# Kernel optimization log

Measured on AMD Instinct MI355X. Metric: run time of the kernel, lower is better.

The kernel has to match this reference:

```python
import jax, jax.numpy as jnp
import numpy as np

N_CLASSES = 64
K_NEIGHBORS = 10
ITERATIONS = 3
IN_DIM = 512
D_MODEL = 256
N_SUPPORT = 2048
N_QUERY = 6144


def setup_inputs() -> dict:
    key = jax.random.key(0)
    k1, k2, k3, k4 = jax.random.split(key, 4)
    support = jax.random.normal(k1, (1, N_SUPPORT, IN_DIM), dtype=jnp.float32)
    query = jax.random.normal(k2, (1, N_QUERY, IN_DIM), dtype=jnp.float32)
    support_labels = jax.random.randint(k3, (N_SUPPORT,), 0, N_CLASSES)
    W = jax.random.normal(k4, (IN_DIM, D_MODEL), dtype=jnp.float32) / np.sqrt(IN_DIM)
    return {"support": support, "query": query, "support_labels": support_labels, "W": W}


def reference(support, query, support_labels, W):
    n_way = N_CLASSES
    ns = support.shape[1]
    nq = query.shape[1]

    # encoder: linear projection
    s_emb = jnp.einsum('bnd,de->bne', support, W)   # (1, ns, D)
    q_emb = jnp.einsum('bnd,de->bne', query, W)     # (1, nq, D)
    all_emb = jnp.concatenate([s_emb, q_emb], axis=1)  # (1, n, D)

    # prototypes (computed in the original forward; unused downstream)
    onehot_s = jax.nn.one_hot(support_labels, n_way, dtype=s_emb.dtype)  # (ns, C)
    counts = onehot_s.sum(0)
    protos = (onehot_s.T @ s_emb[0]) / jnp.maximum(counts, 1.0)[:, None]

    # kNN graph via cdist + topk(smallest) + scatter
    x = all_emb[0]                                  # (n, D)
    n = x.shape[0]
    sq = jnp.sum(x * x, axis=-1)
    d2 = sq[:, None] + sq[None, :] - 2.0 * (x @ x.T)
    dist = jnp.sqrt(jnp.maximum(d2, 0.0))           # (n, n)
    k = min(K_NEIGHBORS, n - 1)
    _, idx = jax.lax.top_k(-dist, k)                # k nearest (incl. self)
    adj = jnp.zeros((n, n), dtype=jnp.float32)
    adj = adj.at[jnp.arange(n)[:, None], idx].set(1.0)
    adj = ((adj + adj.T) > 0).astype(jnp.float32)   # symmetrize

    # row-normalized transition and label propagation
    deg = adj.sum(axis=1, keepdims=True)
    deg = jnp.where(deg == 0, 1.0, deg)
    trans = adj / deg
    label_mat = jnp.concatenate(
        [onehot_s, jnp.zeros((nq, n_way), dtype=jnp.float32)], axis=0)  # (n, C)
    labels = label_mat
    for _ in range(ITERATIONS):
        labels = trans @ labels

    pred = jnp.argmax(labels, axis=-1)              # (n,)
    query_pred = pred[ns:]
    logits = jax.nn.one_hot(query_pred, n_way, dtype=jnp.float32)[None]  # (1, nq, C)
    # protos participates in the original forward; keep it live (no-op add of zeros)
    logits = logits + 0.0 * jnp.sum(protos) * 0.0
    return logits
```

## Files before the change

kernel.cpp:

```cpp
#include <hip/hip_runtime.h>
#include <stdint.h>

#define NS   2048
#define NQ   6144
#define NN   8192
#define IND  512
#define DM   256
#define KNB  10
#define NSPLIT 8
#define PCAP 1536

#define AS1 __attribute__((address_space(1)))
#define AS3 __attribute__((address_space(3)))

typedef short bf16x8 __attribute__((ext_vector_type(8)));
typedef float f32x4  __attribute__((ext_vector_type(4)));
typedef unsigned long long u64;

__device__ __forceinline__ unsigned short f2bf(float v)
{
    unsigned int u = __float_as_uint(v);
    unsigned int r = (u + 0x7fffu + ((u >> 16) & 1u)) >> 16;
    return (unsigned short)r;
}
__device__ __forceinline__ float bf2f(unsigned short h)
{
    return __uint_as_float(((unsigned int)h) << 16);
}

__device__ __forceinline__ void key_insert(u64 key, u64 K[KNB])
{
    u64 cur = key;
#pragma unroll
    for (int s = 0; s < KNB; ++s) {
        u64 lo = (cur < K[s]) ? cur : K[s];
        u64 hi = (cur < K[s]) ? K[s] : cur;
        K[s] = lo; cur = hi;
    }
}

__global__ __launch_bounds__(256) void wpack_kernel(const float* __restrict__ W,
                                                    bf16x8* __restrict__ Wthi,
                                                    bf16x8* __restrict__ Wtlo)
{
    int f = blockIdx.x * 256 + threadIdx.x;
    int dim = f & 255, qp = (f >> 8) & 3, c = f >> 10;
    int k0 = 32 * c + 8 * qp;
    bf16x8 h8, l8;
#pragma unroll
    for (int j = 0; j < 8; ++j) {
        float v = W[(size_t)(k0 + j) * DM + dim];
        unsigned short hu = f2bf(v);
        float hf = bf2f(hu);
        unsigned short lu = f2bf(v - hf);
        h8[j] = (short)hu; l8[j] = (short)lu;
    }
    Wthi[f] = h8; Wtlo[f] = l8;
}

__global__ __launch_bounds__(256) void embed_kernel(
    const float* __restrict__ support, const float* __restrict__ query,
    const bf16x8* __restrict__ Wthi, const bf16x8* __restrict__ Wtlo,
    bf16x8* __restrict__ Ghi, bf16x8* __restrict__ Glo, float* __restrict__ sq)
{
    __shared__ __align__(16) char lds[36928];
    bf16x8* Ehf = reinterpret_cast<bf16x8*>(lds);
    bf16x8* Elf = Ehf + 1024;
    float*  et  = reinterpret_cast<float*>(lds);
    float*  sqred = reinterpret_cast<float*>(lds + 32768);
    const int t = threadIdx.x;
    const int l = t & 63, w = t >> 6;
    const int lm = l & 15, q = l >> 4;
    const int i0 = blockIdx.x * 16;

    {
        const int node = t & 15;
        const int g = i0 + node;
        const float* src = (g < NS) ? (support + (size_t)g * IND)
                                    : (query + (size_t)(g - NS) * IND);
#pragma unroll
        for (int i = 0; i < 4; ++i) {
            int cq = (t >> 4) + 16 * i;
            const float* p = src + cq * 8;
            float4 v0 = *reinterpret_cast<const float4*>(p);
            float4 v1 = *reinterpret_cast<const float4*>(p + 4);
            float vv[8] = {v0.x, v0.y, v0.z, v0.w, v1.x, v1.y, v1.z, v1.w};
            bf16x8 h8, l8;
#pragma unroll
            for (int j = 0; j < 8; ++j) {
                unsigned short hu = f2bf(vv[j]);
                float hf = bf2f(hu);
                unsigned short lu = f2bf(vv[j] - hf);
                h8[j] = (short)hu; l8[j] = (short)lu;
            }
            Ehf[cq * 16 + node] = h8;
            Elf[cq * 16 + node] = l8;
        }
    }
    __syncthreads();

    f32x4 acc[4];
#pragma unroll
    for (int nt = 0; nt < 4; ++nt) acc[nt] = (f32x4){0.f, 0.f, 0.f, 0.f};
    const int dimb = 64 * w + lm;
    for (int c = 0; c < 16; ++c) {
        const bf16x8 Anh = Ehf[(c * 4 + q) * 16 + lm];
        const bf16x8 Anl = Elf[(c * 4 + q) * 16 + lm];
        const int fb = c * 1024 + q * 256 + dimb;
#pragma unroll
        for (int nt = 0; nt < 4; ++nt) {
            const bf16x8 Wh = Wthi[fb + 16 * nt];
            const bf16x8 Wl = Wtlo[fb + 16 * nt];
            f32x4 a = acc[nt];
            a = __builtin_amdgcn_mfma_f32_16x16x32_bf16(Anh, Wh, a, 0, 0, 0);
            a = __builtin_amdgcn_mfma_f32_16x16x32_bf16(Anh, Wl, a, 0, 0, 0);
            a = __builtin_amdgcn_mfma_f32_16x16x32_bf16(Anl, Wh, a, 0, 0, 0);
            a = __builtin_amdgcn_mfma_f32_16x16x32_bf16(Anl, Wl, a, 0, 0, 0);
            acc[nt] = a;
        }
    }
    __syncthreads();

#pragma unroll
    for (int r = 0; r < 4; ++r) {
        float s = 0.f;
#pragma unroll
        for (int nt = 0; nt < 4; ++nt) {
            float v = acc[nt][r];
            et[(4 * q + r) * 260 + dimb + 16 * nt] = v;
            s += v * v;
        }
        sqred[(4 * q + r) * 65 + w * 16 + lm] = s;
    }
    __syncthreads();

#pragma unroll
    for (int i = 0; i < 2; ++i) {
        int f = t + 256 * i;
        int node = f & 15, qd = (f >> 4) & 3, cd = f >> 6;
        const float* ep = &et[node * 260 + 32 * cd + 8 * qd];
        bf16x8 h8, l8;
#pragma unroll
        for (int j = 0; j < 8; ++j) {
            float v = ep[j];
            unsigned short hu = f2bf(v);
            float hf = bf2f(hu);
            unsigned short lu = f2bf(v - hf);
            h8[j] = (short)hu; l8[j] = (short)lu;
        }
        size_t gi = (size_t)(cd * 4 + qd) * NN + i0 + node;
        Ghi[gi] = h8;
        Glo[gi] = l8;
    }
    if (t < 16) {
        float s = 0.f;
#pragma unroll
        for (int x = 0; x < 64; ++x) s += sqred[t * 65 + x];
        sq[i0 + t] = s;
    }
}

__global__ __launch_bounds__(256, 2) void dist_topk_kernel(
    const bf16x8* __restrict__ Ghi, const bf16x8* __restrict__ Glo,
    const float* __restrict__ sq, u64* __restrict__ cand)
{
    __shared__ bf16x8 stage[2][1024];
    __shared__ u64 stk[4][256];
    const int t  = threadIdx.x;
    const int l  = t & 63, w = t >> 6;
    const int lm = l & 15, q = l >> 4;
    const int i0 = blockIdx.x * 64;
    const int row = i0 + 16 * w + lm;
    const int split = blockIdx.y;

    const float  sqi    = sq[row];
    const size_t rowIdx = (size_t)q * NN + row;

    u64 K[KNB];
#pragma unroll
    for (int s = 0; s < KNB; ++s) K[s] = ~0ull;
    u64 thr = ~0ull;
    u64 thr_row = ~0ull;
    int cnt = 0;

    auto drain = [&]() {
        u64 live = __ballot(cnt > 0);
        while (live) {
            if (cnt > 0) {
                --cnt;
                u64 key = stk[cnt][t];
                if (key < thr) {
                    key_insert(key, K);
                    thr = K[KNB - 1];
                }
            }
            live = __ballot(cnt > 0);
        }
    };

    auto stage_issue = [&](int it, int b) {
        const int jt = split * 8 + (it >> 3);
        const int c  = it & 7;
        const int j0 = jt * 128;
        const size_t cbase = (size_t)c * (NN * 4);
        const bool hi = (w < 2);
        const int  wf = (w & 1) * 256;
        const bf16x8* gsel = hi ? Ghi : Glo;
#pragma unroll
        for (int u = 0; u < 4; ++u) {
            const int f  = wf + u * 64;
            const int qr = f >> 7, col0 = f & 127;
            const bf16x8* g = gsel + cbase + (size_t)qr * NN + j0 + col0 + l;
            __builtin_amdgcn_global_load_lds((const AS1 void*)g,
                                             (AS3 void*)&stage[b][(hi ? 0 : 512) + f],
                                             16, 0, 0);
        }
    };

    stage_issue(0, 0);
    __syncthreads();

    f32x4 acc[8];
    for (int it = 0; it < 64; ++it) {
        const int c = it & 7;
        const int b = it & 1;
        if (it + 1 < 64) stage_issue(it + 1, (it + 1) & 1);
        if (c == 0) {
#pragma unroll
            for (int mt = 0; mt < 8; ++mt) acc[mt] = (f32x4){0.f, 0.f, 0.f, 0.f};
        }
        const size_t co = (size_t)c * (NN * 4);
        const bf16x8 Bh = Ghi[co + rowIdx];
        const bf16x8 Bl = Glo[co + rowIdx];
        const bf16x8* sh = &stage[b][0];
        const bf16x8* sl = &stage[b][512];
        const int fq = q * 128 + lm;
#pragma unroll
        for (int mt = 0; mt < 8; ++mt) {
            const int fi = fq + 16 * mt;
            const bf16x8 Ah = sh[fi];
            const bf16x8 Al = sl[fi];
            f32x4 a = acc[mt];
            a = __builtin_amdgcn_mfma_f32_16x16x32_bf16(Ah, Bh, a, 0, 0, 0);
            a = __builtin_amdgcn_mfma_f32_16x16x32_bf16(Ah, Bl, a, 0, 0, 0);
            a = __builtin_amdgcn_mfma_f32_16x16x32_bf16(Al, Bh, a, 0, 0, 0);
            a = __builtin_amdgcn_mfma_f32_16x16x32_bf16(Al, Bl, a, 0, 0, 0);
            acc[mt] = a;
        }
        if (c == 7) {
            const int j0 = split * 1024 + (it >> 3) * 128;
#pragma unroll
            for (int mt = 0; mt < 8; ++mt) {
                const int jb = j0 + 16 * mt + 4 * q;
                const f32x4 sqj = *reinterpret_cast<const f32x4*>(&sq[jb]);
#pragma unroll
                for (int r = 0; r < 4; ++r) {
                    float d2 = fmaxf(sqi + sqj[r] - 2.0f * acc[mt][r], 0.0f);
                    u64 key = ((u64)__float_as_uint(d2) << 32) | (unsigned)(jb + r);
                    if (key < thr_row) { stk[cnt][t] = key; ++cnt; }
                }
                drain();
            }
            u64 tr = K[KNB - 1];
            u64 o  = __shfl_xor(tr, 16, 64); tr = (o < tr) ? o : tr;
            o      = __shfl_xor(tr, 32, 64); tr = (o < tr) ? o : tr;
            thr_row = tr;
        }
        __syncthreads();
    }
    __syncthreads();
    u64* dump = reinterpret_cast<u64*>(&stage[0][0]);
#pragma unroll
    for (int s = 0; s < KNB; ++s) dump[t * KNB + s] = K[s];
    if (q == 0) {
#pragma unroll
        for (int qq = 1; qq < 4; ++qq)
#pragma unroll
            for (int s = 0; s < KNB; ++s) {
                u64 key = dump[(t + qq * 16) * KNB + s];
                if (key < thr) {
                    key_insert(key, K);
                    thr = K[KNB - 1];
                }
            }
        size_t base = (size_t)row * (NSPLIT * KNB) + split * KNB;
#pragma unroll
        for (int s = 0; s < KNB; ++s) cand[base + s] = K[s];
    }
}

__global__ __launch_bounds__(256) void merge_adj_kernel(
    const u64* __restrict__ cand, unsigned int* __restrict__ bits)
{
    int i = blockIdx.x * blockDim.x + threadIdx.x;
    if (i >= NN) return;
    const u64* cp = cand + (size_t)i * (NSPLIT * KNB);
    u64 K[KNB];
#pragma unroll
    for (int s = 0; s < KNB; ++s) K[s] = cp[s];
    u64 thr = K[KNB - 1];
    for (int s = KNB; s < NSPLIT * KNB; ++s) {
        u64 key = cp[s];
        if (key < thr) { key_insert(key, K); thr = K[KNB - 1]; }
    }
#pragma unroll
    for (int s = 0; s < KNB; ++s) {
        int j = (int)(K[s] & 0xFFFFFFFFu);
        atomicOr(&bits[(size_t)i * 256 + (j >> 5)], 1u << (j & 31));
        atomicOr(&bits[(size_t)j * 256 + (i >> 5)], 1u << (i & 31));
    }
}

__device__ __forceinline__ int build_list(const unsigned int* __restrict__ row,
                                          int c, int* __restrict__ lst)
{
    unsigned int mw[4];
#pragma unroll
    for (int k = 0; k < 4; ++k) mw[k] = row[4 * c + k];
    int cnt = __popc(mw[0]) + __popc(mw[1]) + __popc(mw[2]) + __popc(mw[3]);
    int incl = cnt;
#pragma unroll
    for (int d = 1; d < 64; d <<= 1) {
        int nb = __shfl_up(incl, d, 64);
        if (c >= d) incl += nb;
    }
    const int off = incl - cnt;
    const int deg = __shfl(incl, 63, 64);
    if (deg <= PCAP) {
        int p = off;
#pragma unroll
        for (int k = 0; k < 4; ++k) {
            unsigned int m = mw[k];
            while (m) {
                int b = __ffs(m) - 1;
                m &= m - 1;
                lst[p++] = (4 * c + k) * 32 + b;
            }
        }
    }
    return deg;
}

__global__ __launch_bounds__(256) void prop_init_kernel(
    const unsigned int* __restrict__ bits, const int* __restrict__ slab,
    float* __restrict__ lout)
{
    __shared__ int lists[4][PCAP];
    const int grp = threadIdx.x >> 6;
    const int c   = threadIdx.x & 63;
    const int i   = blockIdx.x * 4 + grp;
    const unsigned int* row = bits + (size_t)i * 256;
    const int deg = build_list(row, c, lists[grp]);
    __syncthreads();
    const float tinv = 1.0f / (float)deg;
    float acc = 0.f;
    if (deg <= PCAP) {
        const int* lst = lists[grp];
        for (int d = 0; d < deg; ++d) {
            int j = lst[d];
            float v = (j < NS && slab[j] == c) ? 1.0f : 0.0f;
            acc += __fmul_rn(tinv, v);
        }
    } else {
        for (int w2 = 0; w2 < 256; ++w2) {
            unsigned int m = row[w2];
            while (m) {
                int b = __ffs(m) - 1; m &= m - 1;
                int j = w2 * 32 + b;
                float v = (j < NS && slab[j] == c) ? 1.0f : 0.0f;
                acc += __fmul_rn(tinv, v);
            }
        }
    }
    lout[(size_t)i * 64 + c] = acc;
}

__global__ __launch_bounds__(256) void prop_kernel(
    const unsigned int* __restrict__ bits, const float* __restrict__ lin,
    float* __restrict__ lout)
{
    __shared__ int lists[4][PCAP];
    const int grp = threadIdx.x >> 6;
    const int c   = threadIdx.x & 63;
    const int i   = blockIdx.x * 4 + grp;
    const unsigned int* row = bits + (size_t)i * 256;
    const int deg = build_list(row, c, lists[grp]);
    __syncthreads();
    const float tinv = 1.0f / (float)deg;
    float acc = 0.f;
    if (deg <= PCAP) {
        const int* lst = lists[grp];
        int d = 0;
        for (; d + 4 <= deg; d += 4) {
            int j0 = lst[d], j1 = lst[d + 1], j2 = lst[d + 2], j3 = lst[d + 3];
            float x0 = lin[(size_t)j0 * 64 + c];
            float x1 = lin[(size_t)j1 * 64 + c];
            float x2 = lin[(size_t)j2 * 64 + c];
            float x3 = lin[(size_t)j3 * 64 + c];
            acc += __fmul_rn(tinv, x0);
            acc += __fmul_rn(tinv, x1);
            acc += __fmul_rn(tinv, x2);
            acc += __fmul_rn(tinv, x3);
        }
        for (; d < deg; ++d) {
            int j = lst[d];
            acc += __fmul_rn(tinv, lin[(size_t)j * 64 + c]);
        }
    } else {
        for (int w2 = 0; w2 < 256; ++w2) {
            unsigned int m = row[w2];
            while (m) {
                int b = __ffs(m) - 1; m &= m - 1;
                int j = w2 * 32 + b;
                acc += __fmul_rn(tinv, lin[(size_t)j * 64 + c]);
            }
        }
    }
    lout[(size_t)i * 64 + c] = acc;
}

__global__ __launch_bounds__(256) void prop_argmax_kernel(
    const unsigned int* __restrict__ bits, const float* __restrict__ lin,
    float* __restrict__ out)
{
    __shared__ int lists[4][PCAP];
    const int grp = threadIdx.x >> 6;
    const int c   = threadIdx.x & 63;
    const int qn  = blockIdx.x * 4 + grp;
    const int i   = NS + qn;
    const unsigned int* row = bits + (size_t)i * 256;
    const int deg = build_list(row, c, lists[grp]);
    __syncthreads();
    const float tinv = 1.0f / (float)deg;
    float acc = 0.f;
    if (deg <= PCAP) {
        const int* lst = lists[grp];
        int d = 0;
        for (; d + 4 <= deg; d += 4) {
            int j0 = lst[d], j1 = lst[d + 1], j2 = lst[d + 2], j3 = lst[d + 3];
            float x0 = lin[(size_t)j0 * 64 + c];
            float x1 = lin[(size_t)j1 * 64 + c];
            float x2 = lin[(size_t)j2 * 64 + c];
            float x3 = lin[(size_t)j3 * 64 + c];
            acc += __fmul_rn(tinv, x0);
            acc += __fmul_rn(tinv, x1);
            acc += __fmul_rn(tinv, x2);
            acc += __fmul_rn(tinv, x3);
        }
        for (; d < deg; ++d) {
            int j = lst[d];
            acc += __fmul_rn(tinv, lin[(size_t)j * 64 + c]);
        }
    } else {
        for (int w2 = 0; w2 < 256; ++w2) {
            unsigned int m = row[w2];
            while (m) {
                int b = __ffs(m) - 1; m &= m - 1;
                int j = w2 * 32 + b;
                acc += __fmul_rn(tinv, lin[(size_t)j * 64 + c]);
            }
        }
    }
    float bv = acc; int bi = c;
#pragma unroll
    for (int off = 32; off >= 1; off >>= 1) {
        float ov = __shfl_xor(bv, off, 64);
        int   oi = __shfl_xor(bi, off, 64);
        if (ov > bv || (ov == bv && oi < bi)) { bv = ov; bi = oi; }
    }
    out[(size_t)qn * 64 + c] = (c == bi) ? 1.0f : 0.0f;
}

extern "C" void kernel_launch(void* const* d_in, const int* in_sizes, int n_in,
                              void* d_out, int out_size, void* d_ws, size_t ws_size,
                              hipStream_t stream)
{
    const float* support = (const float*)d_in[0];
    const float* query   = (const float*)d_in[1];
    const int*   slab    = (const int*)d_in[2];
    const float* W       = (const float*)d_in[3];
    float* out = (float*)d_out;
    char*  ws  = (char*)d_ws;

    const size_t GHI_OFF = 0;
    const size_t GLO_OFF = 4194304;
    const size_t SQ_OFF  = 8388608;
    const size_t CV_OFF  = 8421376;
    const size_t CI_OFF  = CV_OFF + (size_t)NN * NSPLIT * KNB * 4;

    bf16x8*       Ghi  = (bf16x8*)(ws + GHI_OFF);
    bf16x8*       Glo  = (bf16x8*)(ws + GLO_OFF);
    unsigned int* bits = (unsigned int*)(ws + GHI_OFF);
    float*        sq   = (float*)(ws + SQ_OFF);
    bf16x8*       Wthi = (bf16x8*)(ws + CV_OFF);
    bf16x8*       Wtlo = (bf16x8*)(ws + CV_OFF + 262144);
    u64*          cand = (u64*)  (ws + CV_OFF);
    float*        la   = (float*)(ws + CV_OFF);
    float*        lb   = (float*)(ws + CI_OFF);

    wpack_kernel<<<64, 256, 0, stream>>>(W, Wthi, Wtlo);
    embed_kernel<<<512, 256, 0, stream>>>(support, query, Wthi, Wtlo, Ghi, Glo, sq);
    dist_topk_kernel<<<dim3(128, NSPLIT), 256, 0, stream>>>(Ghi, Glo, sq, cand);
    hipMemsetAsync(bits, 0, (size_t)NN * 256 * sizeof(unsigned int), stream);
    merge_adj_kernel<<<NN / 256, 256, 0, stream>>>(cand, bits);
    prop_init_kernel<<<NN / 4, 256, 0, stream>>>(bits, slab, lb);
    prop_kernel<<<NN / 4, 256, 0, stream>>>(bits, lb, la);
    prop_argmax_kernel<<<NQ / 4, 256, 0, stream>>>(bits, la, out);
}
```

Baseline: 464.2 us.

## Fuse adjacency build and label propagation into one cooperative grid-synced kernel

Replaces the memset, merge_adj, prop_init, prop and prop_argmax launches with a single persistent cooperative kernel of 512 blocks. The phases are separated by grid-wide syncs, and each block loops over its share of rows. The intent is to remove the per-launch overhead and the idle gaps between the small dependent stages. In exchange it runs fewer resident blocks per phase and adds grid barrier cost. If the cooperative launch fails, it falls back to the original multi-kernel path.

```diff
diff --git a/kernel.cpp b/kernel.cpp
--- a/kernel.cpp
+++ b/kernel.cpp
@@ -1,5 +1,8 @@
 #include <hip/hip_runtime.h>
+#include <hip/hip_cooperative_groups.h>
 #include <stdint.h>
+
+namespace cg = cooperative_groups;
 
 #define NS   2048
 #define NQ   6144
@@ -289,28 +292,6 @@
     }
 }
 
-__global__ __launch_bounds__(256) void merge_adj_kernel(
-    const u64* __restrict__ cand, unsigned int* __restrict__ bits)
-{
-    int i = blockIdx.x * blockDim.x + threadIdx.x;
-    if (i >= NN) return;
-    const u64* cp = cand + (size_t)i * (NSPLIT * KNB);
-    u64 K[KNB];
-#pragma unroll
-    for (int s = 0; s < KNB; ++s) K[s] = cp[s];
-    u64 thr = K[KNB - 1];
-    for (int s = KNB; s < NSPLIT * KNB; ++s) {
-        u64 key = cp[s];
-        if (key < thr) { key_insert(key, K); thr = K[KNB - 1]; }
-    }
-#pragma unroll
-    for (int s = 0; s < KNB; ++s) {
-        int j = (int)(K[s] & 0xFFFFFFFFu);
-        atomicOr(&bits[(size_t)i * 256 + (j >> 5)], 1u << (j & 31));
-        atomicOr(&bits[(size_t)j * 256 + (i >> 5)], 1u << (i & 31));
-    }
-}
-
 __device__ __forceinline__ int build_list(const unsigned int* __restrict__ row,
                                           int c, int* __restrict__ lst)
 {
@@ -341,55 +322,14 @@
     return deg;
 }
 
-__global__ __launch_bounds__(256) void prop_init_kernel(
-    const unsigned int* __restrict__ bits, const int* __restrict__ slab,
-    float* __restrict__ lout)
-{
-    __shared__ int lists[4][PCAP];
-    const int grp = threadIdx.x >> 6;
-    const int c   = threadIdx.x & 63;
-    const int i   = blockIdx.x * 4 + grp;
-    const unsigned int* row = bits + (size_t)i * 256;
-    const int deg = build_list(row, c, lists[grp]);
-    __syncthreads();
+__device__ __forceinline__ float prop_gather(const unsigned int* __restrict__ row,
+                                             int c, int* __restrict__ lst,
+                                             const float* __restrict__ lin)
+{
+    const int deg = build_list(row, c, lst);
     const float tinv = 1.0f / (float)deg;
     float acc = 0.f;
     if (deg <= PCAP) {
-        const int* lst = lists[grp];
-        for (int d = 0; d < deg; ++d) {
-            int j = lst[d];
-            float v = (j < NS && slab[j] == c) ? 1.0f : 0.0f;
-            acc += __fmul_rn(tinv, v);
-        }
-    } else {
-        for (int w2 = 0; w2 < 256; ++w2) {
-            unsigned int m = row[w2];
-            while (m) {
-                int b = __ffs(m) - 1; m &= m - 1;
-                int j = w2 * 32 + b;
-                float v = (j < NS && slab[j] == c) ? 1.0f : 0.0f;
-                acc += __fmul_rn(tinv, v);
-            }
-        }
-    }
-    lout[(size_t)i * 64 + c] = acc;
-}
-
-__global__ __launch_bounds__(256) void prop_kernel(
-    const unsigned int* __restrict__ bits, const float* __restrict__ lin,
-    float* __restrict__ lout)
-{
-    __shared__ int lists[4][PCAP];
-    const int grp = threadIdx.x >> 6;
-    const int c   = threadIdx.x & 63;
-    const int i   = blockIdx.x * 4 + grp;
-    const unsigned int* row = bits + (size_t)i * 256;
-    const int deg = build_list(row, c, lists[grp]);
-    __syncthreads();
-    const float tinv = 1.0f / (float)deg;
-    float acc = 0.f;
-    if (deg <= PCAP) {
-        const int* lst = lists[grp];
         int d = 0;
         for (; d + 4 <= deg; d += 4) {
             int j0 = lst[d], j1 = lst[d + 1], j2 = lst[d + 2], j3 = lst[d + 3];
@@ -416,7 +356,160 @@
             }
         }
     }
-    lout[(size_t)i * 64 + c] = acc;
+    return acc;
+}
+
+__device__ __forceinline__ float prop_init_body(const unsigned int* __restrict__ row,
+                                                int c, int* __restrict__ lst,
+                                                const int* __restrict__ slab)
+{
+    const int deg = build_list(row, c, lst);
+    const float tinv = 1.0f / (float)deg;
+    float acc = 0.f;
+    if (deg <= PCAP) {
+        for (int d = 0; d < deg; ++d) {
+            int j = lst[d];
+            float v = (j < NS && slab[j] == c) ? 1.0f : 0.0f;
+            acc += __fmul_rn(tinv, v);
+        }
+    } else {
+        for (int w2 = 0; w2 < 256; ++w2) {
+            unsigned int m = row[w2];
+            while (m) {
+                int b = __ffs(m) - 1; m &= m - 1;
+                int j = w2 * 32 + b;
+                float v = (j < NS && slab[j] == c) ? 1.0f : 0.0f;
+                acc += __fmul_rn(tinv, v);
+            }
+        }
+    }
+    return acc;
+}
+
+__global__ __launch_bounds__(256) void graph_tail_kernel(
+    const u64* __restrict__ cand, const int* __restrict__ slab,
+    unsigned int* __restrict__ bits, float* __restrict__ la,
+    float* __restrict__ lb, float* __restrict__ out)
+{
+    cg::grid_group g = cg::this_grid();
+    __shared__ int lists[4][PCAP];
+    const int t   = threadIdx.x;
+    const int grp = t >> 6;
+    const int c   = t & 63;
+
+    {
+        uint4* p = reinterpret_cast<uint4*>(bits) + (size_t)blockIdx.x * 1024 + t * 4;
+        p[0] = (uint4){0u, 0u, 0u, 0u};
+        p[1] = (uint4){0u, 0u, 0u, 0u};
+        p[2] = (uint4){0u, 0u, 0u, 0u};
+        p[3] = (uint4){0u, 0u, 0u, 0u};
+    }
+    __threadfence();
+    g.sync();
+    __threadfence();
+
+    if (t < 16) {
+        const int i = blockIdx.x * 16 + t;
+        const u64* cp = cand + (size_t)i * (NSPLIT * KNB);
+        u64 K[KNB];
+#pragma unroll
+        for (int s = 0; s < KNB; ++s) K[s] = cp[s];
+        u64 thr = K[KNB - 1];
+        for (int s = KNB; s < NSPLIT * KNB; ++s) {
+            u64 key = cp[s];
+            if (key < thr) { key_insert(key, K); thr = K[KNB - 1]; }
+        }
+#pragma unroll
+        for (int s = 0; s < KNB; ++s) {
+            int j = (int)(K[s] & 0xFFFFFFFFu);
+            atomicOr(&bits[(size_t)i * 256 + (j >> 5)], 1u << (j & 31));
+            atomicOr(&bits[(size_t)j * 256 + (i >> 5)], 1u << (i & 31));
+        }
+    }
+    __threadfence();
+    g.sync();
+    __threadfence();
+
+    for (int rep = 0; rep < 4; ++rep) {
+        const int i = rep * 2048 + blockIdx.x * 4 + grp;
+        const unsigned int* row = bits + (size_t)i * 256;
+        lb[(size_t)i * 64 + c] = prop_init_body(row, c, lists[grp], slab);
+    }
+    __threadfence();
+    g.sync();
+    __threadfence();
+
+    for (int rep = 0; rep < 4; ++rep) {
+        const int i = rep * 2048 + blockIdx.x * 4 + grp;
+        const unsigned int* row = bits + (size_t)i * 256;
+        la[(size_t)i * 64 + c] = prop_gather(row, c, lists[grp], lb);
+    }
+    __threadfence();
+    g.sync();
+    __threadfence();
+
+    for (int rep = 0; rep < 3; ++rep) {
+        const int qn = rep * 2048 + blockIdx.x * 4 + grp;
+        if (qn < NQ) {
+            const int i = NS + qn;
+            const unsigned int* row = bits + (size_t)i * 256;
+            float acc = prop_gather(row, c, lists[grp], la);
+            float bv = acc; int bi = c;
+#pragma unroll
+            for (int off = 32; off >= 1; off >>= 1) {
+                float ov = __shfl_xor(bv, off, 64);
+                int   oi = __shfl_xor(bi, off, 64);
+                if (ov > bv || (ov == bv && oi < bi)) { bv = ov; bi = oi; }
+            }
+            out[(size_t)qn * 64 + c] = (c == bi) ? 1.0f : 0.0f;
+        }
+    }
+}
+
+__global__ __launch_bounds__(256) void merge_adj_kernel(
+    const u64* __restrict__ cand, unsigned int* __restrict__ bits)
+{
+    int i = blockIdx.x * blockDim.x + threadIdx.x;
+    if (i >= NN) return;
+    const u64* cp = cand + (size_t)i * (NSPLIT * KNB);
+    u64 K[KNB];
+#pragma unroll
+    for (int s = 0; s < KNB; ++s) K[s] = cp[s];
+    u64 thr = K[KNB - 1];
+    for (int s = KNB; s < NSPLIT * KNB; ++s) {
+        u64 key = cp[s];
+        if (key < thr) { key_insert(key, K); thr = K[KNB - 1]; }
+    }
+#pragma unroll
+    for (int s = 0; s < KNB; ++s) {
+        int j = (int)(K[s] & 0xFFFFFFFFu);
+        atomicOr(&bits[(size_t)i * 256 + (j >> 5)], 1u << (j & 31));
+        atomicOr(&bits[(size_t)j * 256 + (i >> 5)], 1u << (i & 31));
+    }
+}
+
+__global__ __launch_bounds__(256) void prop_init_kernel(
+    const unsigned int* __restrict__ bits, const int* __restrict__ slab,
+    float* __restrict__ lout)
+{
+    __shared__ int lists[4][PCAP];
+    const int grp = threadIdx.x >> 6;
+    const int c   = threadIdx.x & 63;
+    const int i   = blockIdx.x * 4 + grp;
+    const unsigned int* row = bits + (size_t)i * 256;
+    lout[(size_t)i * 64 + c] = prop_init_body(row, c, lists[grp], slab);
+}
+
+__global__ __launch_bounds__(256) void prop_kernel(
+    const unsigned int* __restrict__ bits, const float* __restrict__ lin,
+    float* __restrict__ lout)
+{
+    __shared__ int lists[4][PCAP];
+    const int grp = threadIdx.x >> 6;
+    const int c   = threadIdx.x & 63;
+    const int i   = blockIdx.x * 4 + grp;
+    const unsigned int* row = bits + (size_t)i * 256;
+    lout[(size_t)i * 64 + c] = prop_gather(row, c, lists[grp], lin);
 }
 
 __global__ __launch_bounds__(256) void prop_argmax_kernel(
@@ -429,38 +522,7 @@
     const int qn  = blockIdx.x * 4 + grp;
     const int i   = NS + qn;
     const unsigned int* row = bits + (size_t)i * 256;
-    const int deg = build_list(row, c, lists[grp]);
-    __syncthreads();
-    const float tinv = 1.0f / (float)deg;
-    float acc = 0.f;
-    if (deg <= PCAP) {
-        const int* lst = lists[grp];
-        int d = 0;
-        for (; d + 4 <= deg; d += 4) {
-            int j0 = lst[d], j1 = lst[d + 1], j2 = lst[d + 2], j3 = lst[d + 3];
-            float x0 = lin[(size_t)j0 * 64 + c];
-            float x1 = lin[(size_t)j1 * 64 + c];
-            float x2 = lin[(size_t)j2 * 64 + c];
-            float x3 = lin[(size_t)j3 * 64 + c];
-            acc += __fmul_rn(tinv, x0);
-            acc += __fmul_rn(tinv, x1);
-            acc += __fmul_rn(tinv, x2);
-            acc += __fmul_rn(tinv, x3);
-        }
-        for (; d < deg; ++d) {
-            int j = lst[d];
-            acc += __fmul_rn(tinv, lin[(size_t)j * 64 + c]);
-        }
-    } else {
-        for (int w2 = 0; w2 < 256; ++w2) {
-            unsigned int m = row[w2];
-            while (m) {
-                int b = __ffs(m) - 1; m &= m - 1;
-                int j = w2 * 32 + b;
-                acc += __fmul_rn(tinv, lin[(size_t)j * 64 + c]);
-            }
-        }
-    }
+    float acc = prop_gather(row, c, lists[grp], lin);
     float bv = acc; int bi = c;
 #pragma unroll
     for (int off = 32; off >= 1; off >>= 1) {
@@ -501,9 +563,16 @@
     wpack_kernel<<<64, 256, 0, stream>>>(W, Wthi, Wtlo);
     embed_kernel<<<512, 256, 0, stream>>>(support, query, Wthi, Wtlo, Ghi, Glo, sq);
     dist_topk_kernel<<<dim3(128, NSPLIT), 256, 0, stream>>>(Ghi, Glo, sq, cand);
-    hipMemsetAsync(bits, 0, (size_t)NN * 256 * sizeof(unsigned int), stream);
-    merge_adj_kernel<<<NN / 256, 256, 0, stream>>>(cand, bits);
-    prop_init_kernel<<<NN / 4, 256, 0, stream>>>(bits, slab, lb);
-    prop_kernel<<<NN / 4, 256, 0, stream>>>(bits, lb, la);
-    prop_argmax_kernel<<<NQ / 4, 256, 0, stream>>>(bits, la, out);
-}
+
+    void* args[] = {(void*)&cand, (void*)&slab, (void*)&bits,
+                    (void*)&la, (void*)&lb, (void*)&out};
+    hipError_t cerr = hipLaunchCooperativeKernel((const void*)graph_tail_kernel,
+                                                 dim3(512), dim3(256), args, 0, stream);
+    if (cerr != hipSuccess) {
+        hipMemsetAsync(bits, 0, (size_t)NN * 256 * sizeof(unsigned int), stream);
+        merge_adj_kernel<<<NN / 256, 256, 0, stream>>>(cand, bits);
+        prop_init_kernel<<<NN / 4, 256, 0, stream>>>(bits, slab, lb);
+        prop_kernel<<<NN / 4, 256, 0, stream>>>(bits, lb, la);
+        prop_argmax_kernel<<<NQ / 4, 256, 0, stream>>>(bits, la, out);
+    }
+}
```

After: 1.011 ms. 118% more time.
